# Kernel tuning notes

Measured on AMD Instinct MI355X. Metric: run time of the kernel, lower is better.

Reference implementation:

```python
import jax, jax.numpy as jnp
import numpy as np

N, E, IN, OUT = 50000, 800000, 256, 256
EPS = 1e-5


def setup_inputs() -> dict:
    key = jax.random.key(0)
    k1, k2, k3 = jax.random.split(key, 3)
    x = jax.random.normal(k1, (N, IN), dtype=jnp.float32)
    edge_index = jax.random.randint(k2, (2, E), 0, N, dtype=jnp.int64)
    batch = jnp.zeros((N,), dtype=jnp.int64)
    # glorot-style init for GCN weight
    scale = jnp.sqrt(2.0 / (IN + OUT)).astype(jnp.float32)
    W = jax.random.normal(k3, (IN, OUT), dtype=jnp.float32) * scale
    conv_bias = jnp.zeros((OUT,), dtype=jnp.float32)
    ln_weight = jnp.ones((OUT,), dtype=jnp.float32)
    ln_bias = jnp.zeros((OUT,), dtype=jnp.float32)
    prelu_a = jnp.full((1,), 0.25, dtype=jnp.float32)  # nn.PReLU default
    return {"x": x, "edge_index": edge_index, "batch": batch, "W": W,
            "conv_bias": conv_bias, "ln_weight": ln_weight,
            "ln_bias": ln_bias, "prelu_a": prelu_a}


def reference(x, edge_index, batch, W, conv_bias, ln_weight, ln_bias, prelu_a):
    n = x.shape[0]
    src, dst = edge_index[0], edge_index[1]
    # GCNConv: add self-loops, symmetric deg^{-1/2} normalization
    loop = jnp.arange(n, dtype=src.dtype)
    src_f = jnp.concatenate([src, loop])  # [E+N]
    dst_f = jnp.concatenate([dst, loop])
    h = x @ W  # [N, OUT] -- transform before propagate (PyG order)
    deg = jax.ops.segment_sum(jnp.ones_like(dst_f, dtype=h.dtype), dst_f,
                              num_segments=n)  # >=1 due to self loops
    dinv = jax.lax.rsqrt(deg)
    norm = dinv[src_f] * dinv[dst_f]  # [E+N]
    out = jax.ops.segment_sum(h[src_f] * norm[:, None], dst_f,
                              num_segments=n) + conv_bias  # [N, OUT]
    # PyG LayerNorm, mode='graph', batch=None: normalize over ALL nodes+feats
    mu = out.mean()
    xc = out - mu
    std = jnp.sqrt((xc * xc).mean())
    y = xc / (std + EPS) * ln_weight + ln_bias
    # PReLU (single shared slope)
    return jnp.where(y >= 0, y, prelu_a * y)
```

## Files before the change

### kernel.cpp

```cpp
#include <hip/hip_runtime.h>
#include <hip/hip_bf16.h>


#define F 256
#define EPSV 1e-5f

typedef __attribute__((ext_vector_type(8))) short short8;
typedef __attribute__((ext_vector_type(4))) float f32x4;

__device__ __forceinline__ unsigned short f2bf(float f) {
  union { float f; unsigned u; } v; v.f = f;
  unsigned r = v.u + 0x7fffu + ((v.u >> 16) & 1u);
  return (unsigned short)(r >> 16);
}

__device__ __forceinline__ float bf2f(unsigned short u) {
  union { unsigned u; float f; } v; v.u = ((unsigned)u) << 16; return v.f;
}


__global__ void count_rank(const int* __restrict__ dst, int* __restrict__ deg_cnt,
                           int* __restrict__ rank, int E, int eb,
                           const float* __restrict__ W, unsigned short* __restrict__ Wb) {
  if ((int)blockIdx.x < eb) {
    int e = blockIdx.x * 256 + threadIdx.x;
    if (e < E) rank[e] = atomicAdd(&deg_cnt[dst[e]], 1);
    return;
  }
  int gid = (blockIdx.x - eb) * 256 + threadIdx.x;
  int j = gid & 7;
  int lane = (gid >> 3) & 63;
  int kc = (gid >> 9) & 7;
  int tt = gid >> 12;
  int k = kc * 32 + (lane >> 4) * 8 + j;
  int n = tt * 16 + (lane & 15);
  Wb[gid] = f2bf(W[k * 256 + n]);
}


__global__ void block_sums(const int* __restrict__ deg_cnt, int* __restrict__ bsum,
                           float* __restrict__ dinv, int N) {
  __shared__ int s[256];
  int t = threadIdx.x;
  int i = blockIdx.x * 256 + t;
  int d = (i < N) ? deg_cnt[i] : 0;
  if (i < N) dinv[i] = rsqrtf((float)(d + 1));
  s[t] = d;
  __syncthreads();
  for (int off = 128; off > 0; off >>= 1) {
    if (t < off) s[t] += s[t + off];
    __syncthreads();
  }
  if (t == 0) bsum[blockIdx.x] = s[0];
}

__global__ void scan_bsums(const int* __restrict__ bsum, int* __restrict__ boff, int nb) {
  __shared__ int s[256];
  int t = threadIdx.x;
  int v = (t < nb) ? bsum[t] : 0;
  s[t] = v;
  __syncthreads();
  for (int off = 1; off < 256; off <<= 1) {
    int x = (t >= off) ? s[t - off] : 0;
    __syncthreads();
    s[t] += x;
    __syncthreads();
  }
  if (t < nb) boff[t] = s[t] - v;
}

__global__ void write_csr(const int* __restrict__ deg_cnt, const int* __restrict__ boff,
                          int* __restrict__ csr_ptr, int N, int E) {
  __shared__ int s[256];
  int t = threadIdx.x;
  int i = blockIdx.x * 256 + t;
  int v = (i < N) ? deg_cnt[i] : 0;
  s[t] = v;
  __syncthreads();
  for (int off = 1; off < 256; off <<= 1) {
    int x = (t >= off) ? s[t - off] : 0;
    __syncthreads();
    s[t] += x;
    __syncthreads();
  }
  if (i < N) csr_ptr[i] = boff[blockIdx.x] + s[t] - v;
  if (i == 0) csr_ptr[N] = E;
}


__global__ void fill_gemm(const int* __restrict__ src, const int* __restrict__ dst,
                          const int* __restrict__ rank, const int* __restrict__ csr_ptr,
                          int* __restrict__ csr_src, int E, int eb,
                          const float* __restrict__ x, const unsigned short* __restrict__ Wb,
                          const float* __restrict__ dinv, ushort4* __restrict__ hb, int N) {
  __shared__ unsigned short lds[16][264];

  if ((int)blockIdx.x < eb) {
    int e = blockIdx.x * 256 + threadIdx.x;
    if (e < E) {
      int d = dst[e];
      csr_src[csr_ptr[d] + rank[e]] = src[e];
    }
    return;
  }

  int bid = blockIdx.x - eb;
  int lane = threadIdx.x & 63;
  int wave = threadIdx.x >> 6;
  int m0 = bid * 16;
  int q = lane >> 4;

  int row = m0 + (lane & 15);
  int rowc = row < N ? row : N - 1;

  f32x4 acc[4] = {{0,0,0,0},{0,0,0,0},{0,0,0,0},{0,0,0,0}};

  for (int kc = 0; kc < 8; ++kc) {
    int koff = kc * 32 + q * 8;
    const float4* xp = (const float4*)(x + (size_t)rowc * F + koff);
    float4 a0 = xp[0];
    float4 a1 = xp[1];
    short8 a;
    a[0] = f2bf(a0.x); a[1] = f2bf(a0.y); a[2] = f2bf(a0.z); a[3] = f2bf(a0.w);
    a[4] = f2bf(a1.x); a[5] = f2bf(a1.y); a[6] = f2bf(a1.z); a[7] = f2bf(a1.w);
#pragma unroll
    for (int tt = 0; tt < 4; ++tt) {
      const short8 b = *(const short8*)(Wb + (((wave * 4 + tt) * 8 + kc) * 64 + lane) * 8);
      acc[tt] = __builtin_amdgcn_mfma_f32_16x16x32_bf16(a, b, acc[tt], 0, 0, 0);
    }
  }

  int crow = q * 4;
  int ccol = lane & 15;
#pragma unroll
  for (int rr = 0; rr < 4; ++rr) {
    int orow = m0 + crow + rr;
    float dv = (orow < N) ? dinv[orow] : 0.f;
#pragma unroll
    for (int tt = 0; tt < 4; ++tt) {
      lds[crow + rr][wave * 64 + tt * 16 + ccol] = f2bf(acc[tt][rr] * dv);
    }
  }
  __syncthreads();
  int t = threadIdx.x;
  int lrow = t >> 4;
  int grow = m0 + lrow;
  if (grow < N) {
#pragma unroll
    for (int it = 0; it < 4; ++it) {
      int c4 = (t & 15) + 16 * it;
      ushort4 u = *(const ushort4*)&lds[lrow][c4 * 4];
      hb[(size_t)grow * 64 + c4] = u;
    }
  }
}


__global__ void aggregate(const ushort4* __restrict__ hb, const int* __restrict__ csr_ptr,
                          const int* __restrict__ csr_src, const float* __restrict__ dinv,
                          const float* __restrict__ conv_bias, float4* __restrict__ out,
                          double2* __restrict__ partials, int N) {
  int wave = threadIdx.x >> 6;
  int lane = threadIdx.x & 63;
  int row = blockIdx.x * 4 + wave;
  float s1 = 0.f, s2 = 0.f;

  if (row < N) {
    float di = dinv[row];
    int b0 = csr_ptr[row], b1 = csr_ptr[row + 1];
    ushort4 self = hb[(size_t)row * 64 + lane];
    float4 acc;
    acc.x = bf2f(self.x); acc.y = bf2f(self.y);
    acc.z = bf2f(self.z); acc.w = bf2f(self.w);

    for (int e = b0; e < b1; e += 16) {
      int idx[16];
#pragma unroll
      for (int j = 0; j < 16; ++j) {
        int ee = e + j;
        idx[j] = csr_src[ee < b1 ? ee : b1 - 1];
      }
      ushort4 v[16];
#pragma unroll
      for (int j = 0; j < 16; ++j) v[j] = hb[(size_t)idx[j] * 64 + lane];
#pragma unroll
      for (int j = 0; j < 16; ++j) {
        float m = (e + j < b1) ? 1.f : 0.f;
        acc.x = fmaf(bf2f(v[j].x), m, acc.x);
        acc.y = fmaf(bf2f(v[j].y), m, acc.y);
        acc.z = fmaf(bf2f(v[j].z), m, acc.z);
        acc.w = fmaf(bf2f(v[j].w), m, acc.w);
      }
    }

    float4 b = *(const float4*)(conv_bias + lane * 4);
    acc.x = fmaf(acc.x, di, b.x);
    acc.y = fmaf(acc.y, di, b.y);
    acc.z = fmaf(acc.z, di, b.z);
    acc.w = fmaf(acc.w, di, b.w);
    out[(size_t)row * 64 + lane] = acc;
    s1 = acc.x + acc.y + acc.z + acc.w;
    s2 = acc.x * acc.x + acc.y * acc.y + acc.z * acc.z + acc.w * acc.w;
  }

  __shared__ float r1[256];
  __shared__ float r2[256];
  int t = threadIdx.x;
  r1[t] = s1;
  r2[t] = s2;
  __syncthreads();
  for (int off = 128; off > 0; off >>= 1) {
    if (t < off) { r1[t] += r1[t + off]; r2[t] += r2[t + off]; }
    __syncthreads();
  }
  if (t == 0) {
    double2 pp;
    pp.x = (double)r1[0];
    pp.y = (double)r2[0];
    partials[blockIdx.x] = pp;
  }
}

__global__ void finalize_stats(const double2* __restrict__ partials, int nb,
                               float* __restrict__ stats, double cnt) {
  __shared__ double q1[1024];
  __shared__ double q2[1024];
  int t = threadIdx.x;
  double a1 = 0.0, a2 = 0.0;
  for (int i = t; i < nb; i += 1024) {
    double2 pp = partials[i];
    a1 += pp.x;
    a2 += pp.y;
  }
  q1[t] = a1;
  q2[t] = a2;
  __syncthreads();
  for (int off = 512; off > 0; off >>= 1) {
    if (t < off) { q1[t] += q1[t + off]; q2[t] += q2[t + off]; }
    __syncthreads();
  }
  if (t == 0) {
    double mu = q1[0] / cnt;
    double var = q2[0] / cnt - mu * mu;
    if (var < 0) var = 0;
    double sd = sqrt(var);
    stats[0] = (float)mu;
    stats[1] = (float)(1.0 / (sd + (double)EPSV));
  }
}

__global__ void norm_prelu(float4* __restrict__ out, const float* __restrict__ stats,
                           const float* __restrict__ lw, const float* __restrict__ lb,
                           const float* __restrict__ pa, int n4) {
  int i = blockIdx.x * blockDim.x + threadIdx.x;
  if (i >= n4) return;
  float mu = stats[0];
  float inv = stats[1];
  float a = pa[0];
  int c4 = (i & 63) * 4;
  float4 w = *(const float4*)(lw + c4);
  float4 b = *(const float4*)(lb + c4);
  float4 v = out[i];
  float y0 = (v.x - mu) * inv * w.x + b.x;
  float y1 = (v.y - mu) * inv * w.y + b.y;
  float y2 = (v.z - mu) * inv * w.z + b.z;
  float y3 = (v.w - mu) * inv * w.w + b.w;
  v.x = y0 >= 0.f ? y0 : a * y0;
  v.y = y1 >= 0.f ? y1 : a * y1;
  v.z = y2 >= 0.f ? y2 : a * y2;
  v.w = y3 >= 0.f ? y3 : a * y3;
  out[i] = v;
}


extern "C" void kernel_launch(void* const* d_in, const int* in_sizes, int n_in,
                              void* d_out, int out_size, void* d_ws, size_t ws_size,
                              hipStream_t stream) {
  const float* x = (const float*)d_in[0];
  const int* eidx = (const int*)d_in[1];
  const float* W = (const float*)d_in[3];
  const float* conv_bias = (const float*)d_in[4];
  const float* ln_w = (const float*)d_in[5];
  const float* ln_b = (const float*)d_in[6];
  const float* prelu_a = (const float*)d_in[7];
  float* out = (float*)d_out;

  int N = in_sizes[0] / F;
  int E = in_sizes[1] / 2;
  const int* src = eidx;
  const int* dst = eidx + E;

  int nAggBlocks = (N + 3) / 4;
  int eb = (E + 255) / 256;
  int gemmb = (N + 15) / 16;
  int NB = (N + 255) / 256;

  char* p = (char*)d_ws;
  auto carve = [&](size_t bytes) { char* r = p; p += (bytes + 255) & ~(size_t)255; return r; };
  ushort4* hb    = (ushort4*)carve((size_t)N * 64 * sizeof(ushort4));
  unsigned short* Wb = (unsigned short*)carve((size_t)F * F * sizeof(short));
  int* deg_cnt   = (int*)carve((size_t)N * sizeof(int));
  int* rank      = (int*)carve((size_t)E * sizeof(int));
  float* dinv    = (float*)carve((size_t)N * sizeof(float));
  int* csr_ptr   = (int*)carve((size_t)(N + 1) * sizeof(int));
  int* csr_src   = (int*)carve((size_t)E * sizeof(int));
  int* bsum      = (int*)carve((size_t)NB * sizeof(int));
  int* boff      = (int*)carve((size_t)NB * sizeof(int));
  double2* partials = (double2*)carve((size_t)nAggBlocks * sizeof(double2));
  float* stats   = (float*)carve(2 * sizeof(float));

  hipMemsetAsync(deg_cnt, 0, (size_t)N * sizeof(int), stream);

  count_rank<<<eb + 256, 256, 0, stream>>>(dst, deg_cnt, rank, E, eb, W, Wb);
  block_sums<<<NB, 256, 0, stream>>>(deg_cnt, bsum, dinv, N);
  scan_bsums<<<1, 256, 0, stream>>>(bsum, boff, NB);
  write_csr<<<NB, 256, 0, stream>>>(deg_cnt, boff, csr_ptr, N, E);
  fill_gemm<<<eb + gemmb, 256, 0, stream>>>(src, dst, rank, csr_ptr, csr_src, E, eb,
                                            x, Wb, dinv, hb, N);
  aggregate<<<nAggBlocks, 256, 0, stream>>>(hb, csr_ptr, csr_src, dinv,
                                            conv_bias, (float4*)out, partials, N);
  finalize_stats<<<1, 1024, 0, stream>>>(partials, nAggBlocks, stats,
                                         (double)N * (double)F);
  int n4 = N * (F / 4);
  norm_prelu<<<(n4 + 255) / 256, 256, 0, stream>>>((float4*)out, stats, ln_w, ln_b, prelu_a, n4);
}
```

Before: 291.3 us.

## Slice feature table into 8 column slabs and split aggregation by slab

The bf16 transformed-feature table is now written as 8 column slices of 32 features each, stored slice-major and with non-temporal stores. Aggregation launches 8x more blocks, one per (row group, slice), and each wave handles 8 edges at once with 8 lanes per edge, followed by a cross-lane shuffle reduction. The aim is to keep each slice's gather working set small enough to stay in cache and to raise memory-level parallelism. The cost is that every block re-reads csr_ptr and csr_src 8 times, partial sums are now kept in float instead of double, and 8x more partials are produced.

```diff
diff --git a/kernel.cpp b/kernel.cpp
--- a/kernel.cpp
+++ b/kernel.cpp
@@ -7,6 +7,7 @@
 
 typedef __attribute__((ext_vector_type(8))) short short8;
 typedef __attribute__((ext_vector_type(4))) float f32x4;
+typedef __attribute__((ext_vector_type(4))) unsigned short us4;
 
 __device__ __forceinline__ unsigned short f2bf(float f) {
   union { float f; unsigned u; } v; v.f = f;
@@ -92,7 +93,7 @@
                           const int* __restrict__ rank, const int* __restrict__ csr_ptr,
                           int* __restrict__ csr_src, int E, int eb,
                           const float* __restrict__ x, const unsigned short* __restrict__ Wb,
-                          const float* __restrict__ dinv, ushort4* __restrict__ hb, int N) {
+                          const float* __restrict__ dinv, us4* __restrict__ hbs, int N) {
   __shared__ unsigned short lds[16][264];
 
   if ((int)blockIdx.x < eb) {
@@ -149,88 +150,98 @@
 #pragma unroll
     for (int it = 0; it < 4; ++it) {
       int c4 = (t & 15) + 16 * it;
-      ushort4 u = *(const ushort4*)&lds[lrow][c4 * 4];
-      hb[(size_t)grow * 64 + c4] = u;
-    }
-  }
-}
-
-
-__global__ void aggregate(const ushort4* __restrict__ hb, const int* __restrict__ csr_ptr,
+      us4 u = *(const us4*)&lds[lrow][c4 * 4];
+      int sl = c4 >> 3, cc = c4 & 7;
+      __builtin_nontemporal_store(u, &hbs[((size_t)sl * N + grow) * 8 + cc]);
+    }
+  }
+}
+
+
+__global__ void aggregate(const us4* __restrict__ hbs, const int* __restrict__ csr_ptr,
                           const int* __restrict__ csr_src, const float* __restrict__ dinv,
-                          const float* __restrict__ conv_bias, float4* __restrict__ out,
-                          double2* __restrict__ partials, int N) {
+                          const float4* __restrict__ conv_bias4, f32x4* __restrict__ out4,
+                          float2* __restrict__ partials, int N) {
+  int sl = blockIdx.x & 7;
+  int rb = blockIdx.x >> 3;
   int wave = threadIdx.x >> 6;
   int lane = threadIdx.x & 63;
-  int row = blockIdx.x * 4 + wave;
-  float s1 = 0.f, s2 = 0.f;
+  int j = lane >> 3;
+  int c = lane & 7;
+  int row = rb * 4 + wave;
+  float ps1 = 0.f, ps2 = 0.f;
 
   if (row < N) {
+    const us4* tab = hbs + (size_t)sl * N * 8;
+    int b0 = csr_ptr[row], b1 = csr_ptr[row + 1];
+    float ax = 0.f, ay = 0.f, az = 0.f, aw = 0.f;
+
+    for (int e = b0; e < b1; e += 16) {
+      int e0 = e + j, e1 = e + 8 + j;
+      int i0 = __builtin_nontemporal_load(csr_src + (e0 < b1 ? e0 : b1 - 1));
+      int i1 = __builtin_nontemporal_load(csr_src + (e1 < b1 ? e1 : b1 - 1));
+      us4 v0 = tab[(size_t)i0 * 8 + c];
+      us4 v1 = tab[(size_t)i1 * 8 + c];
+      float m0 = (e0 < b1) ? 1.f : 0.f;
+      float m1 = (e1 < b1) ? 1.f : 0.f;
+      ax = fmaf(bf2f(v0.x), m0, ax); ay = fmaf(bf2f(v0.y), m0, ay);
+      az = fmaf(bf2f(v0.z), m0, az); aw = fmaf(bf2f(v0.w), m0, aw);
+      ax = fmaf(bf2f(v1.x), m1, ax); ay = fmaf(bf2f(v1.y), m1, ay);
+      az = fmaf(bf2f(v1.z), m1, az); aw = fmaf(bf2f(v1.w), m1, aw);
+    }
+
+#pragma unroll
+    for (int off = 8; off <= 32; off <<= 1) {
+      ax += __shfl_xor(ax, off, 64);
+      ay += __shfl_xor(ay, off, 64);
+      az += __shfl_xor(az, off, 64);
+      aw += __shfl_xor(aw, off, 64);
+    }
+
+    us4 sv = tab[(size_t)row * 8 + c];
+    ax += bf2f(sv.x); ay += bf2f(sv.y); az += bf2f(sv.z); aw += bf2f(sv.w);
     float di = dinv[row];
-    int b0 = csr_ptr[row], b1 = csr_ptr[row + 1];
-    ushort4 self = hb[(size_t)row * 64 + lane];
-    float4 acc;
-    acc.x = bf2f(self.x); acc.y = bf2f(self.y);
-    acc.z = bf2f(self.z); acc.w = bf2f(self.w);
-
-    for (int e = b0; e < b1; e += 16) {
-      int idx[16];
-#pragma unroll
-      for (int j = 0; j < 16; ++j) {
-        int ee = e + j;
-        idx[j] = csr_src[ee < b1 ? ee : b1 - 1];
-      }
-      ushort4 v[16];
-#pragma unroll
-      for (int j = 0; j < 16; ++j) v[j] = hb[(size_t)idx[j] * 64 + lane];
-#pragma unroll
-      for (int j = 0; j < 16; ++j) {
-        float m = (e + j < b1) ? 1.f : 0.f;
-        acc.x = fmaf(bf2f(v[j].x), m, acc.x);
-        acc.y = fmaf(bf2f(v[j].y), m, acc.y);
-        acc.z = fmaf(bf2f(v[j].z), m, acc.z);
-        acc.w = fmaf(bf2f(v[j].w), m, acc.w);
-      }
-    }
-
-    float4 b = *(const float4*)(conv_bias + lane * 4);
-    acc.x = fmaf(acc.x, di, b.x);
-    acc.y = fmaf(acc.y, di, b.y);
-    acc.z = fmaf(acc.z, di, b.z);
-    acc.w = fmaf(acc.w, di, b.w);
-    out[(size_t)row * 64 + lane] = acc;
-    s1 = acc.x + acc.y + acc.z + acc.w;
-    s2 = acc.x * acc.x + acc.y * acc.y + acc.z * acc.z + acc.w * acc.w;
+    float4 b = conv_bias4[sl * 8 + c];
+    f32x4 y;
+    y.x = fmaf(ax, di, b.x);
+    y.y = fmaf(ay, di, b.y);
+    y.z = fmaf(az, di, b.z);
+    y.w = fmaf(aw, di, b.w);
+    if (j == 0) {
+      __builtin_nontemporal_store(y, &out4[(size_t)row * 64 + sl * 8 + c]);
+      ps1 = y.x + y.y + y.z + y.w;
+      ps2 = y.x * y.x + y.y * y.y + y.z * y.z + y.w * y.w;
+    }
   }
 
   __shared__ float r1[256];
   __shared__ float r2[256];
   int t = threadIdx.x;
-  r1[t] = s1;
-  r2[t] = s2;
+  r1[t] = ps1;
+  r2[t] = ps2;
   __syncthreads();
   for (int off = 128; off > 0; off >>= 1) {
     if (t < off) { r1[t] += r1[t + off]; r2[t] += r2[t + off]; }
     __syncthreads();
   }
   if (t == 0) {
-    double2 pp;
-    pp.x = (double)r1[0];
-    pp.y = (double)r2[0];
+    float2 pp;
+    pp.x = r1[0];
+    pp.y = r2[0];
     partials[blockIdx.x] = pp;
   }
 }
 
-__global__ void finalize_stats(const double2* __restrict__ partials, int nb,
+__global__ void finalize_stats(const float2* __restrict__ partials, int nb,
                                float* __restrict__ stats, double cnt) {
   __shared__ double q1[1024];
   __shared__ double q2[1024];
   int t = threadIdx.x;
   double a1 = 0.0, a2 = 0.0;
   for (int i = t; i < nb; i += 1024) {
-    double2 pp = partials[i];
-    a1 += pp.x;
-    a2 += pp.y;
+    float2 pp = partials[i];
+    a1 += (double)pp.x;
+    a2 += (double)pp.y;
   }
   q1[t] = a1;
   q2[t] = a2;
@@ -290,14 +301,15 @@
   const int* src = eidx;
   const int* dst = eidx + E;
 
-  int nAggBlocks = (N + 3) / 4;
+  int rowBlocks = (N + 3) / 4;
+  int nAggBlocks = rowBlocks * 8;
   int eb = (E + 255) / 256;
   int gemmb = (N + 15) / 16;
   int NB = (N + 255) / 256;
 
   char* p = (char*)d_ws;
   auto carve = [&](size_t bytes) { char* r = p; p += (bytes + 255) & ~(size_t)255; return r; };
-  ushort4* hb    = (ushort4*)carve((size_t)N * 64 * sizeof(ushort4));
+  us4* hbs       = (us4*)carve((size_t)N * 64 * sizeof(us4));
   unsigned short* Wb = (unsigned short*)carve((size_t)F * F * sizeof(short));
   int* deg_cnt   = (int*)carve((size_t)N * sizeof(int));
   int* rank      = (int*)carve((size_t)E * sizeof(int));
@@ -306,7 +318,7 @@
   int* csr_src   = (int*)carve((size_t)E * sizeof(int));
   int* bsum      = (int*)carve((size_t)NB * sizeof(int));
   int* boff      = (int*)carve((size_t)NB * sizeof(int));
-  double2* partials = (double2*)carve((size_t)nAggBlocks * sizeof(double2));
+  float2* partials = (float2*)carve((size_t)nAggBlocks * sizeof(float2));
   float* stats   = (float*)carve(2 * sizeof(float));
 
   hipMemsetAsync(deg_cnt, 0, (size_t)N * sizeof(int), stream);
@@ -316,9 +328,10 @@
   scan_bsums<<<1, 256, 0, stream>>>(bsum, boff, NB);
   write_csr<<<NB, 256, 0, stream>>>(deg_cnt, boff, csr_ptr, N, E);
   fill_gemm<<<eb + gemmb, 256, 0, stream>>>(src, dst, rank, csr_ptr, csr_src, E, eb,
-                                            x, Wb, dinv, hb, N);
-  aggregate<<<nAggBlocks, 256, 0, stream>>>(hb, csr_ptr, csr_src, dinv,
-                                            conv_bias, (float4*)out, partials, N);
+                                            x, Wb, dinv, hbs, N);
+  aggregate<<<nAggBlocks, 256, 0, stream>>>(hbs, csr_ptr, csr_src, dinv,
+                                            (const float4*)conv_bias, (f32x4*)out,
+                                            partials, N);
   finalize_stats<<<1, 1024, 0, stream>>>(partials, nAggBlocks, stats,
                                          (double)N * (double)F);
   int n4 = N * (F / 4);
```

Result: slower. 425.7 us (+46.1%).
